# Performance work log

Hardware: AMD Instinct MI355X
Metric: run time of the kernel (lower is better)

The kernel has to match this reference:

```python
import jax, jax.numpy as jnp
import numpy as np

DIM = 512
NUM_HEADS = 8
HEAD_DIM = DIM // NUM_HEADS
MAX_SLICES = 1024
SCALE = float(np.sqrt(HEAD_DIM))


def setup_inputs() -> dict:
    key = jax.random.key(0)
    ks = jax.random.split(key, 12)
    B, Nv, Nt, D = 4, 1024, 512, DIM
    std = 0.02
    inp = {
        "visual_tokens": jax.random.normal(ks[0], (B, Nv, D), jnp.float32),
        "text_tokens": jax.random.normal(ks[1], (B, Nt, D), jnp.float32),
        # Linear weights stored as [in, out] (i.e., torch W^T), so y = x @ W + b
        "W_Q": jax.random.normal(ks[2], (D, D), jnp.float32) * std,
        "b_Q": jnp.zeros((D,), jnp.float32),
        "W_K": jax.random.normal(ks[3], (D, D), jnp.float32) * std,
        "b_K": jnp.zeros((D,), jnp.float32),
        "W_V": jax.random.normal(ks[4], (D, D), jnp.float32) * std,
        "b_V": jnp.zeros((D,), jnp.float32),
        "W_O": jax.random.normal(ks[5], (D, D), jnp.float32) * std,
        "b_O": jnp.zeros((D,), jnp.float32),
        "bias_table": jax.random.normal(ks[6], (2 * MAX_SLICES - 1, NUM_HEADS), jnp.float32) * std,
        "ln_gamma": jnp.ones((D,), jnp.float32),
        "ln_beta": jnp.zeros((D,), jnp.float32),
    }
    return inp


def _layernorm(x, gamma, beta, eps=1e-5):
    mu = jnp.mean(x, axis=-1, keepdims=True)
    var = jnp.var(x, axis=-1, keepdims=True)
    return (x - mu) * jax.lax.rsqrt(var + eps) * gamma + beta


def reference(visual_tokens, text_tokens, W_Q, b_Q, W_K, b_K, W_V, b_V, W_O, b_O,
              bias_table, ln_gamma, ln_beta):
    Z = jnp.concatenate([visual_tokens, text_tokens], axis=1)  # [B, N, D]
    B, N, D = Z.shape
    Z = _layernorm(Z, ln_gamma, ln_beta)

    def proj(W, b):
        return (Z @ W + b).reshape(B, N, NUM_HEADS, HEAD_DIM).transpose(0, 2, 1, 3)

    Q = proj(W_Q, b_Q)  # [B, H, N, hd]
    K = proj(W_K, b_K)
    V = proj(W_V, b_V)

    attn = jnp.einsum("bhqd,bhkd->bhqk", Q, K) / SCALE  # [B, H, N, N]

    # relative slice bias: [H, N, N]
    coords = jnp.arange(N)
    rel = coords[:, None] - coords[None, :] + (MAX_SLICES - 1)
    rel = jnp.clip(rel, 0, 2 * MAX_SLICES - 2)
    bias = bias_table[rel]                      # [N, N, H]
    bias = jnp.transpose(bias, (2, 0, 1))[None]  # [1, H, N, N]

    attn = jax.nn.softmax(attn + bias, axis=-1)
    out = jnp.einsum("bhqk,bhkd->bhqd", attn, V)  # [B, H, N, hd]
    out = out.transpose(0, 2, 1, 3).reshape(B, N, D)
    return out @ W_O + b_O
```

## Files before the change

kernel.cpp:

```cpp
#include <hip/hip_runtime.h>
#include <stdint.h>

#define NSEQ   1536
#define NBATCH 4
#define NM     (NBATCH * NSEQ)
#define DMODEL 512
#define NHEAD  8
#define HD     64
#define TBLN   2047

typedef __attribute__((ext_vector_type(4))) float  f32x4;
typedef __attribute__((ext_vector_type(4))) int    i32x4;
typedef __attribute__((ext_vector_type(8))) __bf16 bf16x8;
typedef unsigned short u16;

static_assert(sizeof(bf16x8) == 16, "bf16x8 must be 16B");

__device__ inline u16 f2bf(float f) {
  union { float f; uint32_t u; } v; v.f = f;
  uint32_t u = v.u;
  return (u16)((u + 0x7fffu + ((u >> 16) & 1u)) >> 16);
}

__device__ inline bf16x8 ld_bf8(const u16* p) {
  i32x4 v = *(const i32x4*)p;
  return __builtin_bit_cast(bf16x8, v);
}

__device__ inline f32x4 mfma16(bf16x8 a, bf16x8 b, f32x4 c) {
  return __builtin_amdgcn_mfma_f32_16x16x32_bf16(a, b, c, 0, 0, 0);
}

__device__ inline void gload_lds16(const void* g, void* l) {
  __builtin_amdgcn_global_load_lds(
      (__attribute__((address_space(1))) void*)(g),
      (__attribute__((address_space(3))) void*)(l), 16, 0, 0);
}

__device__ inline uint32_t pkbf(float a, float b) {
  uint32_t r;
  asm("v_cvt_pk_bf16_f32 %0, %1, %2" : "=v"(r) : "v"(a), "v"(b));
  return r;
}

__device__ inline float exp2_raw(float x) {
  float r;
  asm("v_exp_f32 %0, %1" : "=v"(r) : "v"(x));
  return r;
}

__global__ __launch_bounds__(256) void ln_kernel(
    const float* __restrict__ vis, const float* __restrict__ txt,
    const float* __restrict__ gamma, const float* __restrict__ beta,
    u16* __restrict__ zn) {
  const int lane = threadIdx.x & 63;
  const int row  = blockIdx.x * 4 + (threadIdx.x >> 6);
  const int b = row / NSEQ, n = row - b * NSEQ;
  const float* src = (n < 1024) ? (vis + ((size_t)b * 1024 + n) * DMODEL)
                                : (txt + ((size_t)b * 512 + (n - 1024)) * DMODEL);
  const float4* s4 = (const float4*)src;
  float4 x0 = s4[lane], x1 = s4[lane + 64];
  float s = x0.x + x0.y + x0.z + x0.w + x1.x + x1.y + x1.z + x1.w;
  float q = x0.x*x0.x + x0.y*x0.y + x0.z*x0.z + x0.w*x0.w
          + x1.x*x1.x + x1.y*x1.y + x1.z*x1.z + x1.w*x1.w;
  #pragma unroll
  for (int m = 1; m < 64; m <<= 1) { s += __shfl_xor(s, m); q += __shfl_xor(q, m); }
  const float mean = s * (1.0f / 512.0f);
  const float var  = q * (1.0f / 512.0f) - mean * mean;
  const float rstd = rsqrtf(var + 1e-5f);
  const float4* g4 = (const float4*)gamma;
  const float4* b4 = (const float4*)beta;
  float4 g0 = g4[lane], g1 = g4[lane + 64], p0 = b4[lane], p1 = b4[lane + 64];
  u16* dst = zn + (size_t)row * DMODEL;
  ushort4 o0, o1;
  o0.x = f2bf((x0.x - mean) * rstd * g0.x + p0.x);
  o0.y = f2bf((x0.y - mean) * rstd * g0.y + p0.y);
  o0.z = f2bf((x0.z - mean) * rstd * g0.z + p0.z);
  o0.w = f2bf((x0.w - mean) * rstd * g0.w + p0.w);
  o1.x = f2bf((x1.x - mean) * rstd * g1.x + p1.x);
  o1.y = f2bf((x1.y - mean) * rstd * g1.y + p1.y);
  o1.z = f2bf((x1.z - mean) * rstd * g1.z + p1.z);
  o1.w = f2bf((x1.w - mean) * rstd * g1.w + p1.w);
  *(ushort4*)(dst + lane * 4)        = o0;
  *(ushort4*)(dst + (lane + 64) * 4) = o1;
}

__global__ __launch_bounds__(256) void wtrans_kernel(
    const float* __restrict__ WQ, const float* __restrict__ WK,
    const float* __restrict__ WV, const float* __restrict__ WO,
    u16* __restrict__ wqkvt, u16* __restrict__ wot) {
  __shared__ float t[32][33];
  const int m = blockIdx.z;
  const float* W = (m == 0) ? WQ : (m == 1) ? WK : (m == 2) ? WV : WO;
  const int n0 = blockIdx.x * 32, k0 = blockIdx.y * 32;
  const int tx = threadIdx.x & 31, ty = threadIdx.x >> 5;
  #pragma unroll
  for (int j = 0; j < 4; ++j)
    t[ty + j * 8][tx] = W[(size_t)(k0 + ty + j * 8) * DMODEL + n0 + tx];
  __syncthreads();
  u16* out = (m < 3) ? (wqkvt + (size_t)m * DMODEL * DMODEL) : wot;
  #pragma unroll
  for (int j = 0; j < 4; ++j)
    out[(size_t)(n0 + ty + j * 8) * DMODEL + k0 + tx] = f2bf(t[tx][ty + j * 8]);
}

__global__ __launch_bounds__(256) void gemm_qkv(
    const u16* __restrict__ A, const u16* __restrict__ Bt,
    const float* __restrict__ bQ, const float* __restrict__ bK, const float* __restrict__ bV,
    u16* __restrict__ Q, u16* __restrict__ Kk, u16* __restrict__ Vt) {
  __shared__ __align__(16) u16 lat[128 * 64];
  __shared__ __align__(16) u16 lbt[128 * 64];
  const int tid = threadIdx.x, lane = tid & 63, w = tid >> 6;
  const int wr = w >> 1, wc = w & 1;
  const int m0 = blockIdx.y * 128, n0 = blockIdx.x * 128;
  f32x4 acc[4][4] = {};
  for (int kt = 0; kt < 8; ++kt) {
    const int k0 = kt * 64;
    #pragma unroll
    for (int i = 0; i < 4; ++i) {
      int ch = w * 256 + i * 64 + lane;
      int row = ch >> 3, pc = ch & 7;
      int kk = k0 + ((pc ^ (row & 7)) << 3);
      gload_lds16(A  + (size_t)(m0 + row) * DMODEL + kk, lat + (size_t)(w * 256 + i * 64) * 8);
      gload_lds16(Bt + (size_t)(n0 + row) * DMODEL + kk, lbt + (size_t)(w * 256 + i * 64) * 8);
    }
    __syncthreads();
    #pragma unroll
    for (int ks = 0; ks < 2; ++ks) {
      bf16x8 af[4], bfr[4];
      const int cc = ks * 4 + (lane >> 4);
      #pragma unroll
      for (int f = 0; f < 4; ++f) {
        int ra = wr * 64 + f * 16 + (lane & 15);
        af[f]  = ld_bf8(lat + ra * 64 + ((cc ^ (ra & 7)) << 3));
        int rb = wc * 64 + f * 16 + (lane & 15);
        bfr[f] = ld_bf8(lbt + rb * 64 + ((cc ^ (rb & 7)) << 3));
      }
      #pragma unroll
      for (int fr = 0; fr < 4; ++fr)
        #pragma unroll
        for (int fc = 0; fc < 4; ++fc)
          acc[fr][fc] = mfma16(af[fr], bfr[fc], acc[fr][fc]);
    }
    __syncthreads();
  }
  #pragma unroll
  for (int fr = 0; fr < 4; ++fr) {
    const int mbase = m0 + wr * 64 + fr * 16 + ((lane >> 4) << 2);
    const int b = mbase / NSEQ;
    const int nseq = mbase - b * NSEQ;
    #pragma unroll
    for (int fc = 0; fc < 4; ++fc) {
      const int col = n0 + wc * 64 + fc * 16 + (lane & 15);
      const int which = col >> 9;
      const int cw = col & 511;
      const int h = cw >> 6, d = cw & 63;
      const float bias = (which == 0) ? bQ[cw] : (which == 1) ? bK[cw] : bV[cw];
      if (which < 2) {
        u16* dst = ((which == 0) ? Q : Kk) + ((size_t)(b * NHEAD + h) * NSEQ + nseq) * HD + d;
        #pragma unroll
        for (int r = 0; r < 4; ++r) dst[(size_t)r * HD] = f2bf(acc[fr][fc][r] + bias);
      } else {
        ushort4 pv;
        pv.x = f2bf(acc[fr][fc][0] + bias);
        pv.y = f2bf(acc[fr][fc][1] + bias);
        pv.z = f2bf(acc[fr][fc][2] + bias);
        pv.w = f2bf(acc[fr][fc][3] + bias);
        *(ushort4*)(Vt + ((size_t)(b * NHEAD + h) * HD + d) * NSEQ + nseq) = pv;
      }
    }
  }
}

__global__ __launch_bounds__(256) void gemm_oproj(
    const u16* __restrict__ A, const u16* __restrict__ Bt,
    const float* __restrict__ bO, float* __restrict__ out) {
  __shared__ __align__(16) u16 lat[128 * 64];
  __shared__ __align__(16) u16 lbt[128 * 64];
  const int tid = threadIdx.x, lane = tid & 63, w = tid >> 6;
  const int wr = w >> 1, wc = w & 1;
  const int m0 = blockIdx.y * 128, n0 = blockIdx.x * 128;
  f32x4 acc[4][4] = {};
  for (int kt = 0; kt < 8; ++kt) {
    const int k0 = kt * 64;
    #pragma unroll
    for (int i = 0; i < 4; ++i) {
      int ch = w * 256 + i * 64 + lane;
      int row = ch >> 3, pc = ch & 7;
      int kk = k0 + ((pc ^ (row & 7)) << 3);
      gload_lds16(A  + (size_t)(m0 + row) * DMODEL + kk, lat + (size_t)(w * 256 + i * 64) * 8);
      gload_lds16(Bt + (size_t)(n0 + row) * DMODEL + kk, lbt + (size_t)(w * 256 + i * 64) * 8);
    }
    __syncthreads();
    #pragma unroll
    for (int ks = 0; ks < 2; ++ks) {
      bf16x8 af[4], bfr[4];
      const int cc = ks * 4 + (lane >> 4);
      #pragma unroll
      for (int f = 0; f < 4; ++f) {
        int ra = wr * 64 + f * 16 + (lane & 15);
        af[f]  = ld_bf8(lat + ra * 64 + ((cc ^ (ra & 7)) << 3));
        int rb = wc * 64 + f * 16 + (lane & 15);
        bfr[f] = ld_bf8(lbt + rb * 64 + ((cc ^ (rb & 7)) << 3));
      }
      #pragma unroll
      for (int fr = 0; fr < 4; ++fr)
        #pragma unroll
        for (int fc = 0; fc < 4; ++fc)
          acc[fr][fc] = mfma16(af[fr], bfr[fc], acc[fr][fc]);
    }
    __syncthreads();
  }
  #pragma unroll
  for (int fr = 0; fr < 4; ++fr) {
    const int mbase = m0 + wr * 64 + fr * 16 + ((lane >> 4) << 2);
    #pragma unroll
    for (int fc = 0; fc < 4; ++fc) {
      const int col = n0 + wc * 64 + fc * 16 + (lane & 15);
      const float bias = bO[col];
      float* dst = out + (size_t)mbase * DMODEL + col;
      #pragma unroll
      for (int r = 0; r < 4; ++r) dst[(size_t)r * DMODEL] = acc[fr][fc][r] + bias;
    }
  }
}

__global__ __launch_bounds__(384, 2) void attn_kernel(
    const u16* __restrict__ Q, const u16* __restrict__ K,
    const u16* __restrict__ Vt, const float* __restrict__ table,
    u16* __restrict__ O) {
  __shared__ float rblds[3072];
  __shared__ __align__(16) u16 kbuf[3][4096];
  __shared__ __align__(16) u16 vbuf[3][4096];
  __shared__ __align__(16) u16 plds[6][2048];
  const int tid = threadIdx.x, lane = tid & 63, w = tid >> 6;
  const int bid = blockIdx.x;
  const int xcd = bid & 7, idx = bid >> 3;
  const int bh  = xcd * 4 + (idx & 3);
  const int qt  = idx >> 2;
  const int h   = bh & (NHEAD - 1);
  for (int t = tid; t < 3072; t += 384) {
    int src = 2558 - t;
    src = src < 0 ? 0 : (src > 2046 ? 2046 : src);
    rblds[t] = table[(size_t)src * NHEAD + h] * 1.4426950408889634f;
  }

  const int lo16 = lane & 15, g = lane >> 4;
  const int q0 = qt * 192 + w * 32;
  const u16* Qb = Q  + (size_t)bh * NSEQ * HD;
  const u16* Kb = K  + (size_t)bh * NSEQ * HD;
  const u16* Vb = Vt + (size_t)bh * HD * NSEQ;

  const int ch0 = tid, ch1 = tid + 256;
  const int sr0 = ch0 >> 3, sc0 = ((ch0 & 7) ^ (sr0 & 7)) << 3;
  const int sr1 = ch1 >> 3, sc1 = ((ch1 & 7) ^ (sr1 & 7)) << 3;
#define STAGE(buf, k0)                                                        \
  if (tid < 256) {                                                            \
    gload_lds16(Kb + (size_t)((k0) + sr0) * HD + sc0, kbuf[buf] + ch0 * 8);   \
    gload_lds16(Kb + (size_t)((k0) + sr1) * HD + sc1, kbuf[buf] + ch1 * 8);   \
    gload_lds16(Vb + (size_t)sr0 * NSEQ + (k0) + sc0, vbuf[buf] + ch0 * 8);   \
    gload_lds16(Vb + (size_t)sr1 * NSEQ + (k0) + sc1, vbuf[buf] + ch1 * 8);   \
  }

  bf16x8 qf[2][2];
  #pragma unroll
  for (int s = 0; s < 2; ++s)
    #pragma unroll
    for (int kd = 0; kd < 2; ++kd)
      qf[s][kd] = ld_bf8(Qb + (size_t)(q0 + s * 16 + lo16) * HD + kd * 32 + g * 8);

  float l_part[2] = {0.f, 0.f};
  f32x4 acc[2][4] = {};

  char* plb = (char*)plds[w];
  const int pswz  = (lo16 & 7) << 4;
  const int wbase = lo16 * 128;
  const int rswz  = lo16 & 7;
  const float* rbp = rblds + (1535 - q0 - lo16 + 4 * g - 16);
  const float c1 = 0.125f * 1.4426950408889634f;

  STAGE(0, 0);
  __syncthreads();
  int cur = 0;

  for (int kt = 0; kt < 24; ++kt) {
    const int k0 = kt * 64;
    int nxt = cur + 1; if (nxt == 3) nxt = 0;
    if (kt < 23) {
      STAGE(nxt, k0 + 64);
      if (tid < 256) asm volatile("s_waitcnt vmcnt(4)" ::: "memory");
    } else {
      if (tid < 256) asm volatile("s_waitcnt vmcnt(0)" ::: "memory");
    }
    __builtin_amdgcn_s_barrier();
    const u16* kb = kbuf[cur];
    const u16* vb = vbuf[cur];
    float bvg[5][4];
    #pragma unroll
    for (int j = 0; j < 5; ++j)
      #pragma unroll
      for (int r = 0; r < 4; ++r)
        bvg[j][r] = rbp[k0 + 16 * j + r];
    f32x4 st[2][4] = {};
    #pragma unroll
    for (int kc = 0; kc < 4; ++kc) {
      const int row = kc * 16 + lo16;
      const bf16x8 kf0 = ld_bf8(kb + row * 64 + ((g ^ rswz) << 3));
      const bf16x8 kf1 = ld_bf8(kb + row * 64 + (((4 + g) ^ rswz) << 3));
      #pragma unroll
      for (int s = 0; s < 2; ++s) {
        st[s][kc] = mfma16(kf0, qf[s][0], st[s][kc]);
        st[s][kc] = mfma16(kf1, qf[s][1], st[s][kc]);
      }
    }
    #pragma unroll
    for (int s = 0; s < 2; ++s)
      #pragma unroll
      for (int kc = 0; kc < 4; ++kc) {
        #pragma unroll
        for (int r = 0; r < 4; ++r) {
          float p = exp2_raw(__builtin_fmaf(st[s][kc][r], c1, bvg[kc - s + 1][r]));
          st[s][kc][r] = p;
          l_part[s] += p;
        }
        uint2 pr;
        pr.x = pkbf(st[s][kc][0], st[s][kc][1]);
        pr.y = pkbf(st[s][kc][2], st[s][kc][3]);
        *(uint2*)(plb + s * 2048 + wbase + ((kc * 32 + g * 8) ^ pswz)) = pr;
      }
    #pragma unroll
    for (int t = 0; t < 2; ++t) {
      bf16x8 pb[2];
      #pragma unroll
      for (int s = 0; s < 2; ++s)
        pb[s] = ld_bf8((const u16*)(plb + s * 2048 + wbase + ((t * 64 + g * 16) ^ pswz)));
      #pragma unroll
      for (int fc = 0; fc < 4; ++fc) {
        const int row = fc * 16 + lo16;
        const bf16x8 vf = ld_bf8(vb + row * 64 + (((t * 4 + g) ^ rswz) << 3));
        #pragma unroll
        for (int s = 0; s < 2; ++s)
          acc[s][fc] = mfma16(vf, pb[s], acc[s][fc]);
      }
    }
    cur = nxt;
  }
  const int b = bh >> 3;
  #pragma unroll
  for (int s = 0; s < 2; ++s) {
    float l_r = l_part[s];
    l_r += __shfl_xor(l_r, 16);
    l_r += __shfl_xor(l_r, 32);
    const float inv = 1.0f / l_r;
    u16* orow = O + ((size_t)(b * NSEQ + q0 + s * 16 + lo16)) * DMODEL + h * HD;
    #pragma unroll
    for (int fc = 0; fc < 4; ++fc) {
      uint2 o4;
      o4.x = pkbf(acc[s][fc][0] * inv, acc[s][fc][1] * inv);
      o4.y = pkbf(acc[s][fc][2] * inv, acc[s][fc][3] * inv);
      *(uint2*)(orow + fc * 16 + g * 4) = o4;
    }
  }
#undef STAGE
}

extern "C" void kernel_launch(void* const* d_in, const int* in_sizes, int n_in,
                              void* d_out, int out_size, void* d_ws, size_t ws_size,
                              hipStream_t stream) {
  const float* vis   = (const float*)d_in[0];
  const float* txt   = (const float*)d_in[1];
  const float* WQ    = (const float*)d_in[2];
  const float* bQ    = (const float*)d_in[3];
  const float* WK    = (const float*)d_in[4];
  const float* bK    = (const float*)d_in[5];
  const float* WV    = (const float*)d_in[6];
  const float* bV    = (const float*)d_in[7];
  const float* WO    = (const float*)d_in[8];
  const float* bO    = (const float*)d_in[9];
  const float* table = (const float*)d_in[10];
  const float* gamma = (const float*)d_in[11];
  const float* beta  = (const float*)d_in[12];
  float* out = (float*)d_out;

  char* p = (char*)d_ws;
  u16* zn    = (u16*)p; p += (size_t)NM * DMODEL * 2;
  u16* wqkvt = (u16*)p; p += (size_t)3 * DMODEL * DMODEL * 2;
  u16* wot   = (u16*)p; p += (size_t)DMODEL * DMODEL * 2;
  u16* q     = (u16*)p; p += (size_t)NM * DMODEL * 2;
  u16* k     = (u16*)p; p += (size_t)NM * DMODEL * 2;
  u16* vt    = (u16*)p; p += (size_t)NM * DMODEL * 2;
  u16* o     = (u16*)p; p += (size_t)NM * DMODEL * 2;

  hipLaunchKernelGGL(ln_kernel, dim3(NM / 4), dim3(256), 0, stream,
                     vis, txt, gamma, beta, zn);
  hipLaunchKernelGGL(wtrans_kernel, dim3(16, 16, 4), dim3(256), 0, stream,
                     WQ, WK, WV, WO, wqkvt, wot);
  hipLaunchKernelGGL(gemm_qkv, dim3(12, 48), dim3(256), 0, stream,
                     zn, wqkvt, bQ, bK, bV, q, k, vt);
  hipLaunchKernelGGL(attn_kernel, dim3(256), dim3(384), 0, stream,
                     q, k, vt, table, o);
  hipLaunchKernelGGL(gemm_oproj, dim3(4, 48), dim3(256), 0, stream,
                     o, wot, bO, out);
}
```

Baseline: 84.74 us.

## Retile GEMMs for more blocks and double-buffer 128-key attention tiles

The QKV GEMM now uses 128x96 tiles (768 blocks instead of 576) and the output projection uses 64x64 tiles (768 blocks instead of 192), so more blocks are available to fill the CUs. The attention kernel moves from a triple-buffered 64-key pipeline to a double-buffered 128-key pipeline with half as many iterations and barriers. Each tile is processed in two 64-key halves with s_setprio raised around the MFMA sections, and the V layout and swizzle are changed to match the wider tile. The trade-offs are more LDS per block, an extra barrier per iteration, and less reuse per GEMM tile.

Result: no change. 85.01 us (+0.3%).

```diff
diff --git a/kernel.cpp b/kernel.cpp
--- a/kernel.cpp
+++ b/kernel.cpp
@@ -109,37 +109,46 @@
     const float* __restrict__ bQ, const float* __restrict__ bK, const float* __restrict__ bV,
     u16* __restrict__ Q, u16* __restrict__ Kk, u16* __restrict__ Vt) {
   __shared__ __align__(16) u16 lat[128 * 64];
-  __shared__ __align__(16) u16 lbt[128 * 64];
+  __shared__ __align__(16) u16 lbt[96 * 64];
   const int tid = threadIdx.x, lane = tid & 63, w = tid >> 6;
   const int wr = w >> 1, wc = w & 1;
-  const int m0 = blockIdx.y * 128, n0 = blockIdx.x * 128;
-  f32x4 acc[4][4] = {};
+  const int m0 = blockIdx.y * 128, n0 = blockIdx.x * 96;
+  f32x4 acc[4][3] = {};
   for (int kt = 0; kt < 8; ++kt) {
     const int k0 = kt * 64;
     #pragma unroll
     for (int i = 0; i < 4; ++i) {
-      int ch = w * 256 + i * 64 + lane;
+      int ch = tid + 256 * i;
       int row = ch >> 3, pc = ch & 7;
       int kk = k0 + ((pc ^ (row & 7)) << 3);
-      gload_lds16(A  + (size_t)(m0 + row) * DMODEL + kk, lat + (size_t)(w * 256 + i * 64) * 8);
-      gload_lds16(Bt + (size_t)(n0 + row) * DMODEL + kk, lbt + (size_t)(w * 256 + i * 64) * 8);
+      gload_lds16(A + (size_t)(m0 + row) * DMODEL + kk, lat + (size_t)ch * 8);
+    }
+    #pragma unroll
+    for (int i = 0; i < 3; ++i) {
+      int ch = tid + 256 * i;
+      int row = ch >> 3, pc = ch & 7;
+      int kk = k0 + ((pc ^ (row & 7)) << 3);
+      gload_lds16(Bt + (size_t)(n0 + row) * DMODEL + kk, lbt + (size_t)ch * 8);
     }
     __syncthreads();
     #pragma unroll
     for (int ks = 0; ks < 2; ++ks) {
-      bf16x8 af[4], bfr[4];
+      bf16x8 af[4], bfr[3];
       const int cc = ks * 4 + (lane >> 4);
       #pragma unroll
       for (int f = 0; f < 4; ++f) {
         int ra = wr * 64 + f * 16 + (lane & 15);
         af[f]  = ld_bf8(lat + ra * 64 + ((cc ^ (ra & 7)) << 3));
-        int rb = wc * 64 + f * 16 + (lane & 15);
+      }
+      #pragma unroll
+      for (int f = 0; f < 3; ++f) {
+        int rb = wc * 48 + f * 16 + (lane & 15);
         bfr[f] = ld_bf8(lbt + rb * 64 + ((cc ^ (rb & 7)) << 3));
       }
       #pragma unroll
       for (int fr = 0; fr < 4; ++fr)
         #pragma unroll
-        for (int fc = 0; fc < 4; ++fc)
+        for (int fc = 0; fc < 3; ++fc)
           acc[fr][fc] = mfma16(af[fr], bfr[fc], acc[fr][fc]);
     }
     __syncthreads();
@@ -150,8 +159,8 @@
     const int b = mbase / NSEQ;
     const int nseq = mbase - b * NSEQ;
     #pragma unroll
-    for (int fc = 0; fc < 4; ++fc) {
-      const int col = n0 + wc * 64 + fc * 16 + (lane & 15);
+    for (int fc = 0; fc < 3; ++fc) {
+      const int col = n0 + wc * 48 + fc * 16 + (lane & 15);
       const int which = col >> 9;
       const int cw = col & 511;
       const int h = cw >> 6, d = cw & 63;
@@ -175,48 +184,48 @@
 __global__ __launch_bounds__(256) void gemm_oproj(
     const u16* __restrict__ A, const u16* __restrict__ Bt,
     const float* __restrict__ bO, float* __restrict__ out) {
-  __shared__ __align__(16) u16 lat[128 * 64];
-  __shared__ __align__(16) u16 lbt[128 * 64];
+  __shared__ __align__(16) u16 lat[64 * 64];
+  __shared__ __align__(16) u16 lbt[64 * 64];
   const int tid = threadIdx.x, lane = tid & 63, w = tid >> 6;
   const int wr = w >> 1, wc = w & 1;
-  const int m0 = blockIdx.y * 128, n0 = blockIdx.x * 128;
-  f32x4 acc[4][4] = {};
+  const int m0 = blockIdx.y * 64, n0 = blockIdx.x * 64;
+  f32x4 acc[2][2] = {};
   for (int kt = 0; kt < 8; ++kt) {
     const int k0 = kt * 64;
     #pragma unroll
-    for (int i = 0; i < 4; ++i) {
-      int ch = w * 256 + i * 64 + lane;
+    for (int i = 0; i < 2; ++i) {
+      int ch = tid + 256 * i;
       int row = ch >> 3, pc = ch & 7;
       int kk = k0 + ((pc ^ (row & 7)) << 3);
-      gload_lds16(A  + (size_t)(m0 + row) * DMODEL + kk, lat + (size_t)(w * 256 + i * 64) * 8);
-      gload_lds16(Bt + (size_t)(n0 + row) * DMODEL + kk, lbt + (size_t)(w * 256 + i * 64) * 8);
+      gload_lds16(A  + (size_t)(m0 + row) * DMODEL + kk, lat + (size_t)ch * 8);
+      gload_lds16(Bt + (size_t)(n0 + row) * DMODEL + kk, lbt + (size_t)ch * 8);
     }
     __syncthreads();
     #pragma unroll
     for (int ks = 0; ks < 2; ++ks) {
-      bf16x8 af[4], bfr[4];
+      bf16x8 af[2], bfr[2];
       const int cc = ks * 4 + (lane >> 4);
       #pragma unroll
-      for (int f = 0; f < 4; ++f) {
-        int ra = wr * 64 + f * 16 + (lane & 15);
+      for (int f = 0; f < 2; ++f) {
+        int ra = wr * 32 + f * 16 + (lane & 15);
         af[f]  = ld_bf8(lat + ra * 64 + ((cc ^ (ra & 7)) << 3));
-        int rb = wc * 64 + f * 16 + (lane & 15);
+        int rb = wc * 32 + f * 16 + (lane & 15);
         bfr[f] = ld_bf8(lbt + rb * 64 + ((cc ^ (rb & 7)) << 3));
       }
       #pragma unroll
-      for (int fr = 0; fr < 4; ++fr)
-        #pragma unroll
-        for (int fc = 0; fc < 4; ++fc)
+      for (int fr = 0; fr < 2; ++fr)
+        #pragma unroll
+        for (int fc = 0; fc < 2; ++fc)
           acc[fr][fc] = mfma16(af[fr], bfr[fc], acc[fr][fc]);
     }
     __syncthreads();
   }
   #pragma unroll
-  for (int fr = 0; fr < 4; ++fr) {
-    const int mbase = m0 + wr * 64 + fr * 16 + ((lane >> 4) << 2);
-    #pragma unroll
-    for (int fc = 0; fc < 4; ++fc) {
-      const int col = n0 + wc * 64 + fc * 16 + (lane & 15);
+  for (int fr = 0; fr < 2; ++fr) {
+    const int mbase = m0 + wr * 32 + fr * 16 + ((lane >> 4) << 2);
+    #pragma unroll
+    for (int fc = 0; fc < 2; ++fc) {
+      const int col = n0 + wc * 32 + fc * 16 + (lane & 15);
       const float bias = bO[col];
       float* dst = out + (size_t)mbase * DMODEL + col;
       #pragma unroll
@@ -230,9 +239,9 @@
     const u16* __restrict__ Vt, const float* __restrict__ table,
     u16* __restrict__ O) {
   __shared__ float rblds[3072];
-  __shared__ __align__(16) u16 kbuf[3][4096];
-  __shared__ __align__(16) u16 vbuf[3][4096];
-  __shared__ __align__(16) u16 plds[6][2048];
+  __shared__ __align__(16) u16 kbuf[2][8192];
+  __shared__ __align__(16) u16 vbuf[2][8192];
+  __shared__ __align__(16) u16 plds[6][4096];
   const int tid = threadIdx.x, lane = tid & 63, w = tid >> 6;
   const int bid = blockIdx.x;
   const int xcd = bid & 7, idx = bid >> 3;
@@ -251,15 +260,18 @@
   const u16* Kb = K  + (size_t)bh * NSEQ * HD;
   const u16* Vb = Vt + (size_t)bh * HD * NSEQ;
 
-  const int ch0 = tid, ch1 = tid + 256;
-  const int sr0 = ch0 >> 3, sc0 = ((ch0 & 7) ^ (sr0 & 7)) << 3;
-  const int sr1 = ch1 >> 3, sc1 = ((ch1 & 7) ^ (sr1 & 7)) << 3;
-#define STAGE(buf, k0)                                                        \
-  if (tid < 256) {                                                            \
-    gload_lds16(Kb + (size_t)((k0) + sr0) * HD + sc0, kbuf[buf] + ch0 * 8);   \
-    gload_lds16(Kb + (size_t)((k0) + sr1) * HD + sc1, kbuf[buf] + ch1 * 8);   \
-    gload_lds16(Vb + (size_t)sr0 * NSEQ + (k0) + sc0, vbuf[buf] + ch0 * 8);   \
-    gload_lds16(Vb + (size_t)sr1 * NSEQ + (k0) + sc1, vbuf[buf] + ch1 * 8);   \
+#define STAGE2(buf, k0)                                                        \
+  if (tid < 256) {                                                             \
+    _Pragma("unroll")                                                          \
+    for (int i = 0; i < 4; ++i) {                                              \
+      int ch = tid + 256 * i;                                                  \
+      int krow = ch >> 3;                                                      \
+      int kcol = ((ch ^ krow) & 7) << 3;                                       \
+      gload_lds16(Kb + (size_t)((k0) + krow) * HD + kcol, kbuf[buf] + (size_t)ch * 8); \
+      int vrow = ch >> 4;                                                      \
+      int vcg  = (ch & 8) | ((ch ^ vrow) & 7);                                 \
+      gload_lds16(Vb + (size_t)vrow * NSEQ + (k0) + vcg * 8, vbuf[buf] + (size_t)ch * 8); \
+    }                                                                          \
   }
 
   bf16x8 qf[2][2];
@@ -279,70 +291,80 @@
   const float* rbp = rblds + (1535 - q0 - lo16 + 4 * g - 16);
   const float c1 = 0.125f * 1.4426950408889634f;
 
-  STAGE(0, 0);
+  STAGE2(0, 0);
   __syncthreads();
   int cur = 0;
 
-  for (int kt = 0; kt < 24; ++kt) {
-    const int k0 = kt * 64;
-    int nxt = cur + 1; if (nxt == 3) nxt = 0;
-    if (kt < 23) {
-      STAGE(nxt, k0 + 64);
-      if (tid < 256) asm volatile("s_waitcnt vmcnt(4)" ::: "memory");
+  for (int kt = 0; kt < 12; ++kt) {
+    const int k0 = kt * 128;
+    const int nxt = cur ^ 1;
+    if (kt < 11) {
+      STAGE2(nxt, k0 + 128);
+      if (tid < 256) asm volatile("s_waitcnt vmcnt(8)" ::: "memory");
     } else {
       if (tid < 256) asm volatile("s_waitcnt vmcnt(0)" ::: "memory");
     }
     __builtin_amdgcn_s_barrier();
     const u16* kb = kbuf[cur];
     const u16* vb = vbuf[cur];
-    float bvg[5][4];
-    #pragma unroll
-    for (int j = 0; j < 5; ++j)
-      #pragma unroll
-      for (int r = 0; r < 4; ++r)
-        bvg[j][r] = rbp[k0 + 16 * j + r];
-    f32x4 st[2][4] = {};
-    #pragma unroll
-    for (int kc = 0; kc < 4; ++kc) {
-      const int row = kc * 16 + lo16;
-      const bf16x8 kf0 = ld_bf8(kb + row * 64 + ((g ^ rswz) << 3));
-      const bf16x8 kf1 = ld_bf8(kb + row * 64 + (((4 + g) ^ rswz) << 3));
-      #pragma unroll
-      for (int s = 0; s < 2; ++s) {
-        st[s][kc] = mfma16(kf0, qf[s][0], st[s][kc]);
-        st[s][kc] = mfma16(kf1, qf[s][1], st[s][kc]);
-      }
-    }
-    #pragma unroll
-    for (int s = 0; s < 2; ++s)
+    #pragma unroll
+    for (int hh = 0; hh < 2; ++hh) {
+      char* plh = plb + hh * 4096;
+      float bvg[5][4];
+      #pragma unroll
+      for (int j = 0; j < 5; ++j)
+        #pragma unroll
+        for (int r = 0; r < 4; ++r)
+          bvg[j][r] = rbp[k0 + hh * 64 + 16 * j + r];
+      f32x4 st[2][4] = {};
+      __builtin_amdgcn_s_setprio(1);
       #pragma unroll
       for (int kc = 0; kc < 4; ++kc) {
-        #pragma unroll
-        for (int r = 0; r < 4; ++r) {
-          float p = exp2_raw(__builtin_fmaf(st[s][kc][r], c1, bvg[kc - s + 1][r]));
-          st[s][kc][r] = p;
-          l_part[s] += p;
+        const int row = hh * 64 + kc * 16 + lo16;
+        const bf16x8 kf0 = ld_bf8(kb + row * 64 + ((g ^ rswz) << 3));
+        const bf16x8 kf1 = ld_bf8(kb + row * 64 + (((4 + g) ^ rswz) << 3));
+        #pragma unroll
+        for (int s = 0; s < 2; ++s) {
+          st[s][kc] = mfma16(kf0, qf[s][0], st[s][kc]);
+          st[s][kc] = mfma16(kf1, qf[s][1], st[s][kc]);
         }
-        uint2 pr;
-        pr.x = pkbf(st[s][kc][0], st[s][kc][1]);
-        pr.y = pkbf(st[s][kc][2], st[s][kc][3]);
-        *(uint2*)(plb + s * 2048 + wbase + ((kc * 32 + g * 8) ^ pswz)) = pr;
-      }
-    #pragma unroll
-    for (int t = 0; t < 2; ++t) {
-      bf16x8 pb[2];
+      }
+      __builtin_amdgcn_s_setprio(0);
       #pragma unroll
       for (int s = 0; s < 2; ++s)
-        pb[s] = ld_bf8((const u16*)(plb + s * 2048 + wbase + ((t * 64 + g * 16) ^ pswz)));
-      #pragma unroll
-      for (int fc = 0; fc < 4; ++fc) {
-        const int row = fc * 16 + lo16;
-        const bf16x8 vf = ld_bf8(vb + row * 64 + (((t * 4 + g) ^ rswz) << 3));
+        #pragma unroll
+        for (int kc = 0; kc < 4; ++kc) {
+          #pragma unroll
+          for (int r = 0; r < 4; ++r) {
+            float p = exp2_raw(__builtin_fmaf(st[s][kc][r], c1, bvg[kc - s + 1][r]));
+            st[s][kc][r] = p;
+            l_part[s] += p;
+          }
+          uint2 pr;
+          pr.x = pkbf(st[s][kc][0], st[s][kc][1]);
+          pr.y = pkbf(st[s][kc][2], st[s][kc][3]);
+          *(uint2*)(plh + s * 2048 + wbase + ((kc * 32 + g * 8) ^ pswz)) = pr;
+        }
+      __builtin_amdgcn_s_setprio(1);
+      #pragma unroll
+      for (int t = 0; t < 2; ++t) {
+        bf16x8 pb[2];
         #pragma unroll
         for (int s = 0; s < 2; ++s)
-          acc[s][fc] = mfma16(vf, pb[s], acc[s][fc]);
-      }
-    }
+          pb[s] = ld_bf8((const u16*)(plh + s * 2048 + wbase + ((t * 64 + g * 16) ^ pswz)));
+        #pragma unroll
+        for (int fc = 0; fc < 4; ++fc) {
+          const int row = fc * 16 + lo16;
+          const int cl = (hh * 8) | (((t * 4 + g) ^ rswz) & 7);
+          const bf16x8 vf = ld_bf8(vb + row * 128 + cl * 8);
+          #pragma unroll
+          for (int s = 0; s < 2; ++s)
+            acc[s][fc] = mfma16(vf, pb[s], acc[s][fc]);
+        }
+      }
+      __builtin_amdgcn_s_setprio(0);
+    }
+    __builtin_amdgcn_s_barrier();
     cur = nxt;
   }
   const int b = bh >> 3;
@@ -361,7 +383,7 @@
       *(uint2*)(orow + fc * 16 + g * 4) = o4;
     }
   }
-#undef STAGE
+#undef STAGE2
 }
 
 extern "C" void kernel_launch(void* const* d_in, const int* in_sizes, int n_in,
@@ -395,10 +417,10 @@
                      vis, txt, gamma, beta, zn);
   hipLaunchKernelGGL(wtrans_kernel, dim3(16, 16, 4), dim3(256), 0, stream,
                      WQ, WK, WV, WO, wqkvt, wot);
-  hipLaunchKernelGGL(gemm_qkv, dim3(12, 48), dim3(256), 0, stream,
+  hipLaunchKernelGGL(gemm_qkv, dim3(16, 48), dim3(256), 0, stream,
                      zn, wqkvt, bQ, bK, bV, q, k, vt);
   hipLaunchKernelGGL(attn_kernel, dim3(256), dim3(384), 0, stream,
                      q, k, vt, table, o);
-  hipLaunchKernelGGL(gemm_oproj, dim3(4, 48), dim3(256), 0, stream,
+  hipLaunchKernelGGL(gemm_oproj, dim3(8, 96), dim3(256), 0, stream,
                      o, wot, bO, out);
 }
```
